# Optimization experiments

Hardware: AMD Instinct MI355X
Metric: run time of the kernel (lower is better)

## Reference

```python
import jax, jax.numpy as jnp
import numpy as np

N_HEADS = 16
HEAD_DIM = 128


def _rotate_half(x):
    x1, x2 = jnp.split(x, 2, axis=-1)
    return jnp.concatenate((-x2, x1), axis=-1)


def setup_inputs() -> dict:
    key = jax.random.key(0)
    ks = jax.random.split(key, 6)
    B, T, D = 2, 2048, 2048
    d = D // N_HEADS  # 128
    x = jax.random.normal(ks[0], (B, T, D), dtype=jnp.float32)
    # RoPE tables (shape [1,1,T,head_dim]) built as in standard implementations
    inv_freq = 1.0 / (10000.0 ** (jnp.arange(0, d, 2, dtype=jnp.float32) / d))
    ang = jnp.arange(T, dtype=jnp.float32)[:, None] * inv_freq[None, :]  # [T, d/2]
    emb = jnp.concatenate((ang, ang), axis=-1)  # [T, d]
    rope_cos = jnp.cos(emb)[None, None]
    rope_sin = jnp.sin(emb)[None, None]
    qkv_w = jax.random.normal(ks[1], (3 * D, D), dtype=jnp.float32) * (1.0 / np.sqrt(D))
    qkv_b = jnp.zeros((3 * D,), dtype=jnp.float32)
    out_w = jax.random.normal(ks[2], (D, D), dtype=jnp.float32) * (1.0 / np.sqrt(D))
    out_b = jnp.zeros((D,), dtype=jnp.float32)
    return {"x": x, "rope_cos": rope_cos, "rope_sin": rope_sin,
            "qkv_w": qkv_w, "qkv_b": qkv_b, "out_w": out_w, "out_b": out_b}


def reference(x, rope_cos, rope_sin, qkv_w, qkv_b, out_w, out_b):
    B, T, D = x.shape
    H, d = N_HEADS, D // N_HEADS
    # fused QKV projection: [B,T,3D] -> [3,B,H,T,d]
    qkv = (jnp.einsum('btd,ed->bte', x, qkv_w) + qkv_b)
    qkv = qkv.reshape(B, T, 3, H, d).transpose(2, 0, 3, 1, 4)
    q, k, v = qkv[0], qkv[1], qkv[2]
    cos = rope_cos[:, :, :T, :].astype(q.dtype)
    sin = rope_sin[:, :, :T, :].astype(q.dtype)
    q = q * cos + _rotate_half(q) * sin
    k = k * cos + _rotate_half(k) * sin
    # causal SDPA
    scale = 1.0 / jnp.sqrt(jnp.array(d, dtype=q.dtype))
    scores = jnp.einsum('bhqd,bhkd->bhqk', q, k) * scale  # [B,H,T,T]
    causal = jnp.tril(jnp.ones((T, T), dtype=bool))
    scores = jnp.where(causal, scores, jnp.finfo(scores.dtype).min)
    attn = jax.nn.softmax(scores, axis=-1)
    out = jnp.einsum('bhqk,bhkd->bhqd', attn, v)  # [B,H,T,d]
    out = out.transpose(0, 2, 1, 3).reshape(B, T, D)
    return jnp.einsum('btd,ed->bte', out, out_w) + out_b
```

## Files before the change

### kernel.cpp

```cpp
#include <hip/hip_runtime.h>
#include <cstdint>
#include <cstddef>

typedef unsigned short u16;
using bf16x8 = __attribute__((ext_vector_type(8))) short;
using f32x4  = __attribute__((ext_vector_type(4))) float;

#define MFMA16(a, b, c) __builtin_amdgcn_mfma_f32_16x16x32_bf16((a), (b), (c), 0, 0, 0)

__device__ __forceinline__ u16 f2bf(float f) {
  union { float f; unsigned u; } x; x.f = f;
  unsigned r = x.u + 0x7fffu + ((x.u >> 16) & 1u);
  return (u16)(r >> 16);
}
__device__ __forceinline__ float bf2f(u16 h) {
  union { unsigned u; float f; } x; x.u = ((unsigned)h) << 16;
  return x.f;
}
__device__ __forceinline__ void gll16(const void* g, void* l) {
  __builtin_amdgcn_global_load_lds((const __attribute__((address_space(1))) void*)g,
                                   (__attribute__((address_space(3))) void*)l, 16, 0, 0);
}

union U8 { bf16x8 v; u16 u[8]; };

__global__ __launch_bounds__(256) void cvt_kernel(const float* __restrict__ in,
                                                  u16* __restrict__ out, int n4) {
  int i = blockIdx.x * blockDim.x + threadIdx.x;
  if (i >= n4) return;
  float4 v = ((const float4*)in)[i];
  ushort4 o;
  o.x = f2bf(v.x); o.y = f2bf(v.y); o.z = f2bf(v.z); o.w = f2bf(v.w);
  ((ushort4*)out)[i] = o;
}

__global__ __launch_bounds__(512, 2) void gemm_bt256(const u16* __restrict__ A,
                                                     const u16* __restrict__ Bw,
                                                     const float* __restrict__ bias,
                                                     void* __restrict__ Cout,
                                                     int M, int N, int K, int out_bf16) {
  __shared__ u16 As_[2][16384];
  __shared__ u16 Bs_[2][16384];
  const int tid = threadIdx.x;
  const int lane = tid & 63, wave = tid >> 6;
  const int col = lane & 15, quad = lane >> 4;
  const int wr = wave >> 2, wc = wave & 3;
  const int bm = blockIdx.y, bn = blockIdx.x;
  const u16* Ag = A + (size_t)bm * 256 * K;
  const u16* Bg = Bw + (size_t)bn * 256 * K;
  const int srow = tid >> 2;
  const int sslot = tid & 3;
  const int ssw = (sslot ^ ((srow >> 1) & 3)) << 3;
  const size_t g0 = (size_t)srow * K + ssw;
  const size_t g1 = (size_t)(srow + 128) * K + ssw;
  const int swq = (quad ^ ((col >> 1) & 3)) << 3;
  const int aro = (wr * 128 + col) * 32 + swq;
  const int bro = (wc * 64 + col) * 32 + swq;
  u16* const As0 = &As_[0][0]; u16* const As1 = &As_[1][0];
  u16* const Bs0 = &Bs_[0][0]; u16* const Bs1 = &Bs_[1][0];
  f32x4 acc[8][4] = {};
  bf16x8 a[8], bq[2];
  const int NI = K >> 7;

#define STG_A(BUF, KS, KT) do { \
    gll16(Ag + g0 + (KT) + (KS) * 32, (void*)((BUF) + (KS) * 8192 + tid * 8)); \
    gll16(Ag + g1 + (KT) + (KS) * 32, (void*)((BUF) + (KS) * 8192 + 4096 + tid * 8)); } while (0)
#define STG_B(BUF, KS, KT) do { \
    gll16(Bg + g0 + (KT) + (KS) * 32, (void*)((BUF) + (KS) * 8192 + tid * 8)); \
    gll16(Bg + g1 + (KT) + (KS) * 32, (void*)((BUF) + (KS) * 8192 + 4096 + tid * 8)); } while (0)
#define RD_A(BUF, KS) do { _Pragma("unroll") \
    for (int m_ = 0; m_ < 8; m_++) \
      a[m_] = *(const bf16x8*)&(BUF)[(KS) * 8192 + aro + m_ * 512]; } while (0)
#define RD_B(BUF, KS, NH) do { _Pragma("unroll") \
    for (int n_ = 0; n_ < 2; n_++) \
      bq[n_] = *(const bf16x8*)&(BUF)[(KS) * 8192 + bro + ((NH) * 2 + n_) * 512]; } while (0)
#define MM(NH) do { _Pragma("unroll") \
    for (int m_ = 0; m_ < 8; m_++) { _Pragma("unroll") \
      for (int n_ = 0; n_ < 2; n_++) \
        acc[m_][(NH) * 2 + n_] = MFMA16(a[m_], bq[n_], acc[m_][(NH) * 2 + n_]); } } while (0)
#define PH(RDS, STGS, MMS, WT) do { \
    RDS; STGS; \
    __builtin_amdgcn_s_barrier(); \
    asm volatile("s_waitcnt lgkmcnt(0)" ::: "memory"); \
    __builtin_amdgcn_s_setprio(1); \
    MMS; \
    __builtin_amdgcn_s_setprio(0); \
    WT; \
    __builtin_amdgcn_s_barrier(); } while (0)
#define VM6 do { asm volatile("s_waitcnt vmcnt(6)" ::: "memory"); } while (0)
#define VM0 do { asm volatile("s_waitcnt vmcnt(0)" ::: "memory"); } while (0)
#define NOPW do { } while (0)

#define ITER(I, LAST) do { \
    const int kt1_ = ((2 * (I) + 1) << 6), kt2_ = kt1_ + 64, kt3_ = kt2_ + 64; \
    PH({ RD_A(As0, 0); RD_B(Bs0, 0, 0); }, { STG_B(Bs1, 1, kt1_); },                MM(0), NOPW); \
    PH({ RD_B(Bs0, 0, 1); },               { if (!(LAST)) STG_A(As0, 0, kt2_); },   MM(1), NOPW); \
    PH({ RD_A(As0, 1); RD_B(Bs0, 1, 1); }, { if (!(LAST)) STG_B(Bs0, 0, kt2_); },   MM(1), NOPW); \
    PH({ RD_B(Bs0, 1, 0); },               { if (!(LAST)) STG_A(As0, 1, kt2_); },   MM(0), \
       if (LAST) { VM0; } else { VM6; }); \
    PH({ RD_A(As1, 0); RD_B(Bs1, 0, 0); }, { if (!(LAST)) STG_B(Bs0, 1, kt2_); },   MM(0), NOPW); \
    PH({ RD_B(Bs1, 0, 1); },               { if (!(LAST)) STG_A(As1, 0, kt3_); },   MM(1), NOPW); \
    PH({ RD_A(As1, 1); RD_B(Bs1, 1, 1); }, { if (!(LAST)) STG_B(Bs1, 0, kt3_); },   MM(1), NOPW); \
    PH({ RD_B(Bs1, 1, 0); },               { if (!(LAST)) STG_A(As1, 1, kt3_); },   MM(0), \
       if (!(LAST)) { VM6; }); \
  } while (0)

  STG_A(As0, 0, 0);  STG_B(Bs0, 0, 0);  STG_A(As0, 1, 0);  STG_B(Bs0, 1, 0);
  STG_A(As1, 0, 64); STG_B(Bs1, 0, 64); STG_A(As1, 1, 64);
  VM6;
  __builtin_amdgcn_s_barrier();

  for (int i = 0; i < NI - 1; ++i) ITER(i, false);
  ITER(NI - 1, true);

#pragma unroll
  for (int i = 0; i < 8; i++) {
    const int row0 = bm * 256 + wr * 128 + i * 16 + quad * 4;
#pragma unroll
    for (int j = 0; j < 4; j++) {
      const int cn = bn * 256 + wc * 64 + j * 16 + col;
      const float bv = bias[cn];
#pragma unroll
      for (int r = 0; r < 4; r++) {
        float v = acc[i][j][r] + bv;
        size_t off = (size_t)(row0 + r) * N + cn;
        if (out_bf16) ((u16*)Cout)[off] = f2bf(v);
        else          ((float*)Cout)[off] = v;
      }
    }
  }
#undef STG_A
#undef STG_B
#undef RD_A
#undef RD_B
#undef MM
#undef PH
#undef VM6
#undef VM0
#undef NOPW
#undef ITER
}

__global__ __launch_bounds__(512, 2) void gemm_bt128(const u16* __restrict__ A,
                                                     const u16* __restrict__ Bw,
                                                     const float* __restrict__ bias,
                                                     void* __restrict__ Cout,
                                                     int M, int N, int K, int out_bf16) {
  __shared__ u16 As_[2][8192];
  __shared__ u16 Bs_[2][16384];
  const int tid = threadIdx.x;
  const int lane = tid & 63, wave = tid >> 6;
  const int col = lane & 15, quad = lane >> 4;
  const int wr = wave >> 2, wc = wave & 3;
  const int bm = blockIdx.y, bn = blockIdx.x;
  const u16* Ag = A + (size_t)bm * 128 * K;
  const u16* Bg = Bw + (size_t)bn * 256 * K;
  const int srow = tid >> 2;
  const int sslot = tid & 3;
  const int ssw = (sslot ^ ((srow >> 1) & 3)) << 3;
  const size_t g0 = (size_t)srow * K + ssw;
  const size_t g1 = (size_t)(srow + 128) * K + ssw;
  const int swq = (quad ^ ((col >> 1) & 3)) << 3;
  const int aro = (wr * 64 + col) * 32 + swq;
  const int bro = (wc * 64 + col) * 32 + swq;
  u16* const As0 = &As_[0][0]; u16* const As1 = &As_[1][0];
  u16* const Bs0 = &Bs_[0][0]; u16* const Bs1 = &Bs_[1][0];
  f32x4 acc[4][4] = {};
  bf16x8 a[4], bq[2];
  const int NI = K >> 7;

#define STG_A(BUF, KS, KT) do { \
    gll16(Ag + g0 + (KT) + (KS) * 32, (void*)((BUF) + (KS) * 4096 + tid * 8)); } while (0)
#define STG_B(BUF, KS, KT) do { \
    gll16(Bg + g0 + (KT) + (KS) * 32, (void*)((BUF) + (KS) * 8192 + tid * 8)); \
    gll16(Bg + g1 + (KT) + (KS) * 32, (void*)((BUF) + (KS) * 8192 + 4096 + tid * 8)); } while (0)
#define RD_A(BUF, KS) do { _Pragma("unroll") \
    for (int m_ = 0; m_ < 4; m_++) \
      a[m_] = *(const bf16x8*)&(BUF)[(KS) * 4096 + aro + m_ * 512]; } while (0)
#define RD_B(BUF, KS, NH) do { _Pragma("unroll") \
    for (int n_ = 0; n_ < 2; n_++) \
      bq[n_] = *(const bf16x8*)&(BUF)[(KS) * 8192 + bro + ((NH) * 2 + n_) * 512]; } while (0)
#define MM(NH) do { _Pragma("unroll") \
    for (int m_ = 0; m_ < 4; m_++) { _Pragma("unroll") \
      for (int n_ = 0; n_ < 2; n_++) \
        acc[m_][(NH) * 2 + n_] = MFMA16(a[m_], bq[n_], acc[m_][(NH) * 2 + n_]); } } while (0)
#define PH(RDS, STGS, MMS, WT) do { \
    RDS; STGS; \
    __builtin_amdgcn_s_barrier(); \
    asm volatile("s_waitcnt lgkmcnt(0)" ::: "memory"); \
    __builtin_amdgcn_s_setprio(1); \
    MMS; \
    __builtin_amdgcn_s_setprio(0); \
    WT; \
    __builtin_amdgcn_s_barrier(); } while (0)
#define VM4 do { asm volatile("s_waitcnt vmcnt(4)" ::: "memory"); } while (0)
#define VM0 do { asm volatile("s_waitcnt vmcnt(0)" ::: "memory"); } while (0)
#define NOPW do { } while (0)

#define ITER(I, LAST) do { \
    const int kt1_ = ((2 * (I) + 1) << 6), kt2_ = kt1_ + 64, kt3_ = kt2_ + 64; \
    PH({ RD_A(As0, 0); RD_B(Bs0, 0, 0); }, { STG_B(Bs1, 1, kt1_); },                MM(0), NOPW); \
    PH({ RD_B(Bs0, 0, 1); },               { if (!(LAST)) STG_A(As0, 0, kt2_); },   MM(1), NOPW); \
    PH({ RD_A(As0, 1); RD_B(Bs0, 1, 1); }, { if (!(LAST)) STG_B(Bs0, 0, kt2_); },   MM(1), NOPW); \
    PH({ RD_B(Bs0, 1, 0); },               { if (!(LAST)) STG_A(As0, 1, kt2_); },   MM(0), \
       if (LAST) { VM0; } else { VM4; }); \
    PH({ RD_A(As1, 0); RD_B(Bs1, 0, 0); }, { if (!(LAST)) STG_B(Bs0, 1, kt2_); },   MM(0), NOPW); \
    PH({ RD_B(Bs1, 0, 1); },               { if (!(LAST)) STG_A(As1, 0, kt3_); },   MM(1), NOPW); \
    PH({ RD_A(As1, 1); RD_B(Bs1, 1, 1); }, { if (!(LAST)) STG_B(Bs1, 0, kt3_); },   MM(1), NOPW); \
    PH({ RD_B(Bs1, 1, 0); },               { if (!(LAST)) STG_A(As1, 1, kt3_); },   MM(0), \
       if (!(LAST)) { VM4; }); \
  } while (0)

  STG_A(As0, 0, 0);  STG_B(Bs0, 0, 0);  STG_A(As0, 1, 0);  STG_B(Bs0, 1, 0);
  STG_A(As1, 0, 64); STG_B(Bs1, 0, 64); STG_A(As1, 1, 64);
  VM4;
  __builtin_amdgcn_s_barrier();

  for (int i = 0; i < NI - 1; ++i) ITER(i, false);
  ITER(NI - 1, true);

#pragma unroll
  for (int i = 0; i < 4; i++) {
    const int row0 = bm * 128 + wr * 64 + i * 16 + quad * 4;
#pragma unroll
    for (int j = 0; j < 4; j++) {
      const int cn = bn * 256 + wc * 64 + j * 16 + col;
      const float bv = bias[cn];
#pragma unroll
      for (int r = 0; r < 4; r++) {
        float v = acc[i][j][r] + bv;
        size_t off = (size_t)(row0 + r) * N + cn;
        if (out_bf16) ((u16*)Cout)[off] = f2bf(v);
        else          ((float*)Cout)[off] = v;
      }
    }
  }
#undef STG_A
#undef STG_B
#undef RD_A
#undef RD_B
#undef MM
#undef PH
#undef VM4
#undef VM0
#undef NOPW
#undef ITER
}

__global__ __launch_bounds__(256) void rope_kernel(const u16* __restrict__ qkv,
                                                   const float* __restrict__ cosT,
                                                   const float* __restrict__ sinT,
                                                   u16* __restrict__ qo,
                                                   u16* __restrict__ ko,
                                                   u16* __restrict__ vt) {
  __shared__ u16 vs[128 * 72];
  const int bh = blockIdx.x;
  const int b = bh >> 4, h = bh & 15;
  const int tb = blockIdx.y;
  const int tid = threadIdx.x;
  const int tl = tid >> 2;
  const int g = tid & 3;
  const int t = tb * 64 + tl;
  const size_t qrow = ((size_t)(b * 2048 + t)) * 6144 + h * 128;
  const size_t orow = ((size_t)bh * 2048 + t) * 128;
  const int tt = t * 128;
  const int dl = g * 16, dh = 64 + dl;
  const float scale = 0.08838834764831845f;
#pragma unroll
  for (int cch = 0; cch < 2; cch++) {
    const int o8 = cch * 8;
    U8 ql, qh, kl, kh, vl, vh;
    ql.v = *(const bf16x8*)&qkv[qrow + dl + o8];
    qh.v = *(const bf16x8*)&qkv[qrow + dh + o8];
    kl.v = *(const bf16x8*)&qkv[qrow + 2048 + dl + o8];
    kh.v = *(const bf16x8*)&qkv[qrow + 2048 + dh + o8];
    vl.v = *(const bf16x8*)&qkv[qrow + 4096 + dl + o8];
    vh.v = *(const bf16x8*)&qkv[qrow + 4096 + dh + o8];
    float cl[8], ch_[8], sl[8], sh_[8];
    *(float4*)&cl[0]  = *(const float4*)&cosT[tt + dl + o8];
    *(float4*)&cl[4]  = *(const float4*)&cosT[tt + dl + o8 + 4];
    *(float4*)&ch_[0] = *(const float4*)&cosT[tt + dh + o8];
    *(float4*)&ch_[4] = *(const float4*)&cosT[tt + dh + o8 + 4];
    *(float4*)&sl[0]  = *(const float4*)&sinT[tt + dl + o8];
    *(float4*)&sl[4]  = *(const float4*)&sinT[tt + dl + o8 + 4];
    *(float4*)&sh_[0] = *(const float4*)&sinT[tt + dh + o8];
    *(float4*)&sh_[4] = *(const float4*)&sinT[tt + dh + o8 + 4];
    U8 aq, bq, ak, bk;
#pragma unroll
    for (int i = 0; i < 8; i++) {
      float qlf = bf2f(ql.u[i]), qhf = bf2f(qh.u[i]);
      float klf = bf2f(kl.u[i]), khf = bf2f(kh.u[i]);
      aq.u[i] = f2bf((qlf * cl[i]  - qhf * sl[i])  * scale);
      bq.u[i] = f2bf((qhf * ch_[i] + qlf * sh_[i]) * scale);
      ak.u[i] = f2bf(klf * cl[i]  - khf * sl[i]);
      bk.u[i] = f2bf(khf * ch_[i] + klf * sh_[i]);
    }
    *(bf16x8*)&qo[orow + dl + o8] = aq.v;
    *(bf16x8*)&qo[orow + dh + o8] = bq.v;
    *(bf16x8*)&ko[orow + dl + o8] = ak.v;
    *(bf16x8*)&ko[orow + dh + o8] = bk.v;
#pragma unroll
    for (int i = 0; i < 8; i++) {
      vs[(dl + o8 + i) * 72 + tl] = vl.u[i];
      vs[(dh + o8 + i) * 72 + tl] = vh.u[i];
    }
  }
  __syncthreads();
#pragma unroll
  for (int c = 0; c < 4; c++) {
    int idx = c * 256 + tid;
    int dd = idx >> 3, chk = idx & 7;
    bf16x8 vv = *(const bf16x8*)&vs[dd * 72 + chk * 8];
    *(bf16x8*)&vt[((size_t)bh * 128 + dd) * 2048 + tb * 64 + chk * 8] = vv;
  }
}

__global__ __launch_bounds__(256) void attn_kernel(const u16* __restrict__ Q,
                                                   const u16* __restrict__ Kk,
                                                   const u16* __restrict__ Vt,
                                                   u16* __restrict__ O) {
  __shared__ u16 Ks[64 * 136];
  __shared__ u16 Vs[128 * 72];
  __shared__ u16 Ps[4][16 * 72];
  const int L = blockIdx.x;
  const int bh = (L < 256) ? (L >> 4) : 16 + ((L - 256) >> 4);
  const int qtile = (L < 256) ? (15 - (L & 15)) : (L & 15);
  const int b = bh >> 4, h = bh & 15;
  const int qb = qtile * 128;
  const int tid = threadIdx.x, wave = tid >> 6, lane = tid & 63;
  const int col = lane & 15, quad = lane >> 4;
  const int qw0 = qb + wave * 32;
  const int qw1 = qw0 + 16;
  const u16* Qg = Q + (size_t)bh * 2048 * 128;
  const u16* Kg = Kk + (size_t)bh * 2048 * 128;
  const u16* Vg = Vt + (size_t)bh * 128 * 2048;
  bf16x8 qf0[4], qf1[4];
#pragma unroll
  for (int c = 0; c < 4; c++) {
    qf0[c] = *(const bf16x8*)&Qg[(size_t)(qw0 + col) * 128 + c * 32 + quad * 8];
    qf1[c] = *(const bf16x8*)&Qg[(size_t)(qw1 + col) * 128 + c * 32 + quad * 8];
  }
  f32x4 o0[8] = {}, o1[8] = {};
  float ls0[4] = {0.f, 0.f, 0.f, 0.f}, ls1[4] = {0.f, 0.f, 0.f, 0.f};
  const int ntiles = (qb + 128) >> 6;
  const int kr = tid >> 2, kc = (tid & 3) * 8;
  const int vr = tid >> 1, vc = (tid & 1) * 8;
  for (int it = 0; it < ntiles; ++it) {
    const int kt = it << 6;
    __syncthreads();
#pragma unroll
    for (int u = 0; u < 4; u++)
      *(bf16x8*)&Ks[kr * 136 + kc + u * 32] =
          *(const bf16x8*)&Kg[(size_t)(kt + kr) * 128 + kc + u * 32];
#pragma unroll
    for (int u = 0; u < 4; u++)
      *(bf16x8*)&Vs[vr * 72 + vc + u * 16] =
          *(const bf16x8*)&Vg[(size_t)vr * 2048 + kt + vc + u * 16];
    __syncthreads();
    if (kt > qw1 + 15) continue;
    const bool do0 = (kt <= qw0 + 15);
    f32x4 s0[4] = {}, s1[4] = {};
#pragma unroll
    for (int c = 0; c < 4; c++) {
#pragma unroll
      for (int kg = 0; kg < 4; kg++) {
        bf16x8 kf = *(const bf16x8*)&Ks[(kg * 16 + col) * 136 + c * 32 + quad * 8];
        s0[kg] = MFMA16(qf0[c], kf, s0[kg]);
        s1[kg] = MFMA16(qf1[c], kf, s1[kg]);
      }
    }
    u16* pw = Ps[wave];
    if (do0) {
#pragma unroll
      for (int kg = 0; kg < 4; kg++)
#pragma unroll
        for (int r = 0; r < 4; r++) {
          int key = kt + kg * 16 + col, qg = qw0 + quad * 4 + r;
          float p = (key <= qg) ? __expf(s0[kg][r]) : 0.f;
          ls0[r] += p;
          pw[(quad * 4 + r) * 72 + kg * 16 + col] = f2bf(p);
        }
#pragma unroll
      for (int ks = 0; ks < 64; ks += 32) {
        bf16x8 pf = *(const bf16x8*)&pw[col * 72 + ks + quad * 8];
#pragma unroll
        for (int dt = 0; dt < 8; dt++) {
          bf16x8 vf = *(const bf16x8*)&Vs[(dt * 16 + col) * 72 + ks + quad * 8];
          o0[dt] = MFMA16(pf, vf, o0[dt]);
        }
      }
    }
    {
#pragma unroll
      for (int kg = 0; kg < 4; kg++)
#pragma unroll
        for (int r = 0; r < 4; r++) {
          int key = kt + kg * 16 + col, qg = qw1 + quad * 4 + r;
          float p = (key <= qg) ? __expf(s1[kg][r]) : 0.f;
          ls1[r] += p;
          pw[(quad * 4 + r) * 72 + kg * 16 + col] = f2bf(p);
        }
#pragma unroll
      for (int ks = 0; ks < 64; ks += 32) {
        bf16x8 pf = *(const bf16x8*)&pw[col * 72 + ks + quad * 8];
#pragma unroll
        for (int dt = 0; dt < 8; dt++) {
          bf16x8 vf = *(const bf16x8*)&Vs[(dt * 16 + col) * 72 + ks + quad * 8];
          o1[dt] = MFMA16(pf, vf, o1[dt]);
        }
      }
    }
  }
#pragma unroll
  for (int st = 1; st < 16; st <<= 1)
#pragma unroll
    for (int r = 0; r < 4; r++) {
      ls0[r] += __shfl_xor(ls0[r], st);
      ls1[r] += __shfl_xor(ls1[r], st);
    }
#pragma unroll
  for (int r = 0; r < 4; r++) {
    float inv0 = 1.0f / ls0[r], inv1 = 1.0f / ls1[r];
    size_t row0 = ((size_t)(b * 2048 + qw0 + quad * 4 + r)) * 2048 + h * 128;
    size_t row1 = ((size_t)(b * 2048 + qw1 + quad * 4 + r)) * 2048 + h * 128;
#pragma unroll
    for (int dt = 0; dt < 8; dt++) {
      O[row0 + dt * 16 + col] = f2bf(o0[dt][r] * inv0);
      O[row1 + dt * 16 + col] = f2bf(o1[dt][r] * inv1);
    }
  }
}

extern "C" void kernel_launch(void* const* d_in, const int* in_sizes, int n_in,
                              void* d_out, int out_size, void* d_ws, size_t ws_size,
                              hipStream_t stream) {
  const float* x        = (const float*)d_in[0];
  const float* rope_cos = (const float*)d_in[1];
  const float* rope_sin = (const float*)d_in[2];
  const float* qkv_w    = (const float*)d_in[3];
  const float* qkv_b    = (const float*)d_in[4];
  const float* out_w    = (const float*)d_in[5];
  const float* out_b    = (const float*)d_in[6];
  float* out = (float*)d_out;
  u16* ws = (u16*)d_ws;
  u16* xb    = ws;
  u16* wqkvb = xb + 8388608;
  u16* woutb = wqkvb + 12582912;
  u16* qkvb  = woutb + 4194304;
  u16* qb    = qkvb + 25165824;
  u16* kb    = qb + 8388608;
  u16* vtb   = kb + 8388608;
  u16* attnb = xb;

  cvt_kernel<<<8192, 256, 0, stream>>>(x, xb, 2097152);
  cvt_kernel<<<12288, 256, 0, stream>>>(qkv_w, wqkvb, 3145728);
  cvt_kernel<<<4096, 256, 0, stream>>>(out_w, woutb, 1048576);
  gemm_bt256<<<dim3(24, 16), 512, 0, stream>>>(xb, wqkvb, qkv_b, qkvb, 4096, 6144, 2048, 1);
  rope_kernel<<<dim3(32, 32), 256, 0, stream>>>(qkvb, rope_cos, rope_sin, qb, kb, vtb);
  attn_kernel<<<dim3(512, 1), 256, 0, stream>>>(qb, kb, vtb, attnb);
  gemm_bt128<<<dim3(8, 32), 512, 0, stream>>>(attnb, woutb, out_b, out, 4096, 2048, 2048, 0);
}
```

Baseline: 430.1 us.

## Swizzle attention LDS layouts, merge PV loops, fuse three convert kernels

Replaces the padded LDS layouts for K, V and P in the attention kernel with XOR-swizzled unpadded layouts to avoid bank conflicts. It gives each query half its own P buffer so both PV products run in one loop that shares each V fragment read. It also merges the three fp32-to-bf16 conversion launches into one kernel to cut launch overhead. The risks are extra index arithmetic and more live registers from the fused PV loop.

```diff
diff --git a/kernel.cpp b/kernel.cpp
--- a/kernel.cpp
+++ b/kernel.cpp
@@ -24,14 +24,23 @@
 
 union U8 { bf16x8 v; u16 u[8]; };
 
-__global__ __launch_bounds__(256) void cvt_kernel(const float* __restrict__ in,
-                                                  u16* __restrict__ out, int n4) {
+__global__ __launch_bounds__(256) void cvt3_kernel(const float* __restrict__ a,
+                                                   const float* __restrict__ b,
+                                                   const float* __restrict__ c,
+                                                   u16* __restrict__ oa,
+                                                   u16* __restrict__ ob,
+                                                   u16* __restrict__ oc,
+                                                   int n1, int n2, int n3) {
   int i = blockIdx.x * blockDim.x + threadIdx.x;
-  if (i >= n4) return;
-  float4 v = ((const float4*)in)[i];
+  const float* src; u16* dst; int j;
+  if (i < n1)            { src = a; dst = oa; j = i; }
+  else if (i < n1 + n2)  { src = b; dst = ob; j = i - n1; }
+  else if (i < n1 + n2 + n3) { src = c; dst = oc; j = i - n1 - n2; }
+  else return;
+  float4 v = ((const float4*)src)[j];
   ushort4 o;
   o.x = f2bf(v.x); o.y = f2bf(v.y); o.z = f2bf(v.z); o.w = f2bf(v.w);
-  ((ushort4*)out)[i] = o;
+  ((ushort4*)dst)[j] = o;
 }
 
 __global__ __launch_bounds__(512, 2) void gemm_bt256(const u16* __restrict__ A,
@@ -319,9 +328,9 @@
                                                    const u16* __restrict__ Kk,
                                                    const u16* __restrict__ Vt,
                                                    u16* __restrict__ O) {
-  __shared__ u16 Ks[64 * 136];
-  __shared__ u16 Vs[128 * 72];
-  __shared__ u16 Ps[4][16 * 72];
+  __shared__ u16 Ks[64 * 128];
+  __shared__ u16 Vs[128 * 64];
+  __shared__ u16 Ps[4][2048];
   const int L = blockIdx.x;
   const int bh = (L < 256) ? (L >> 4) : 16 + ((L - 256) >> 4);
   const int qtile = (L < 256) ? (15 - (L & 15)) : (L & 15);
@@ -343,19 +352,23 @@
   f32x4 o0[8] = {}, o1[8] = {};
   float ls0[4] = {0.f, 0.f, 0.f, 0.f}, ls1[4] = {0.f, 0.f, 0.f, 0.f};
   const int ntiles = (qb + 128) >> 6;
-  const int kr = tid >> 2, kc = (tid & 3) * 8;
-  const int vr = tid >> 1, vc = (tid & 1) * 8;
+  const int skr = tid >> 4, sks = tid & 15;
+  const int svr = tid >> 1, svc = tid & 1;
   for (int it = 0; it < ntiles; ++it) {
     const int kt = it << 6;
     __syncthreads();
 #pragma unroll
-    for (int u = 0; u < 4; u++)
-      *(bf16x8*)&Ks[kr * 136 + kc + u * 32] =
-          *(const bf16x8*)&Kg[(size_t)(kt + kr) * 128 + kc + u * 32];
-#pragma unroll
-    for (int u = 0; u < 4; u++)
-      *(bf16x8*)&Vs[vr * 72 + vc + u * 16] =
-          *(const bf16x8*)&Vg[(size_t)vr * 2048 + kt + vc + u * 16];
+    for (int u = 0; u < 4; u++) {
+      const int row = u * 16 + skr;
+      *(bf16x8*)&Ks[row * 128 + ((sks ^ (row & 7)) << 3)] =
+          *(const bf16x8*)&Kg[(size_t)(kt + row) * 128 + (sks << 3)];
+    }
+#pragma unroll
+    for (int u = 0; u < 4; u++) {
+      const int ch = svc + 2 * u;
+      *(bf16x8*)&Vs[svr * 64 + ((ch ^ (svr & 7)) << 3)] =
+          *(const bf16x8*)&Vg[(size_t)svr * 2048 + kt + (ch << 3)];
+    }
     __syncthreads();
     if (kt > qw1 + 15) continue;
     const bool do0 = (kt <= qw0 + 15);
@@ -364,12 +377,14 @@
     for (int c = 0; c < 4; c++) {
 #pragma unroll
       for (int kg = 0; kg < 4; kg++) {
-        bf16x8 kf = *(const bf16x8*)&Ks[(kg * 16 + col) * 136 + c * 32 + quad * 8];
+        const int krow = kg * 16 + col;
+        bf16x8 kf = *(const bf16x8*)&Ks[krow * 128 + (((c * 4 + quad) ^ (krow & 7)) << 3)];
         s0[kg] = MFMA16(qf0[c], kf, s0[kg]);
         s1[kg] = MFMA16(qf1[c], kf, s1[kg]);
       }
     }
-    u16* pw = Ps[wave];
+    u16* pw0 = &Ps[wave][0];
+    u16* pw1 = &Ps[wave][1024];
     if (do0) {
 #pragma unroll
       for (int kg = 0; kg < 4; kg++)
@@ -378,17 +393,9 @@
           int key = kt + kg * 16 + col, qg = qw0 + quad * 4 + r;
           float p = (key <= qg) ? __expf(s0[kg][r]) : 0.f;
           ls0[r] += p;
-          pw[(quad * 4 + r) * 72 + kg * 16 + col] = f2bf(p);
+          const int prow = quad * 4 + r;
+          pw0[prow * 64 + (((kg * 2 + (col >> 3)) ^ (prow & 7)) << 3) + (col & 7)] = f2bf(p);
         }
-#pragma unroll
-      for (int ks = 0; ks < 64; ks += 32) {
-        bf16x8 pf = *(const bf16x8*)&pw[col * 72 + ks + quad * 8];
-#pragma unroll
-        for (int dt = 0; dt < 8; dt++) {
-          bf16x8 vf = *(const bf16x8*)&Vs[(dt * 16 + col) * 72 + ks + quad * 8];
-          o0[dt] = MFMA16(pf, vf, o0[dt]);
-        }
-      }
     }
     {
 #pragma unroll
@@ -398,16 +405,22 @@
           int key = kt + kg * 16 + col, qg = qw1 + quad * 4 + r;
           float p = (key <= qg) ? __expf(s1[kg][r]) : 0.f;
           ls1[r] += p;
-          pw[(quad * 4 + r) * 72 + kg * 16 + col] = f2bf(p);
+          const int prow = quad * 4 + r;
+          pw1[prow * 64 + (((kg * 2 + (col >> 3)) ^ (prow & 7)) << 3) + (col & 7)] = f2bf(p);
         }
-#pragma unroll
-      for (int ks = 0; ks < 64; ks += 32) {
-        bf16x8 pf = *(const bf16x8*)&pw[col * 72 + ks + quad * 8];
-#pragma unroll
-        for (int dt = 0; dt < 8; dt++) {
-          bf16x8 vf = *(const bf16x8*)&Vs[(dt * 16 + col) * 72 + ks + quad * 8];
-          o1[dt] = MFMA16(pf, vf, o1[dt]);
-        }
+    }
+#pragma unroll
+    for (int ks = 0; ks < 64; ks += 32) {
+      const int cbase = ks >> 3;
+      bf16x8 pf0, pf1;
+      if (do0) pf0 = *(const bf16x8*)&pw0[col * 64 + (((cbase + quad) ^ (col & 7)) << 3)];
+      pf1 = *(const bf16x8*)&pw1[col * 64 + (((cbase + quad) ^ (col & 7)) << 3)];
+#pragma unroll
+      for (int dt = 0; dt < 8; dt++) {
+        const int vrow = dt * 16 + col;
+        bf16x8 vf = *(const bf16x8*)&Vs[vrow * 64 + (((cbase + quad) ^ (vrow & 7)) << 3)];
+        if (do0) o0[dt] = MFMA16(pf0, vf, o0[dt]);
+        o1[dt] = MFMA16(pf1, vf, o1[dt]);
       }
     }
   }
@@ -452,9 +465,8 @@
   u16* vtb   = kb + 8388608;
   u16* attnb = xb;
 
-  cvt_kernel<<<8192, 256, 0, stream>>>(x, xb, 2097152);
-  cvt_kernel<<<12288, 256, 0, stream>>>(qkv_w, wqkvb, 3145728);
-  cvt_kernel<<<4096, 256, 0, stream>>>(out_w, woutb, 1048576);
+  cvt3_kernel<<<24576, 256, 0, stream>>>(x, qkv_w, out_w, xb, wqkvb, woutb,
+                                         2097152, 3145728, 1048576);
   gemm_bt256<<<dim3(24, 16), 512, 0, stream>>>(xb, wqkvb, qkv_b, qkvb, 4096, 6144, 2048, 1);
   rope_kernel<<<dim3(32, 32), 256, 0, stream>>>(qkvb, rope_cos, rope_sin, qb, kb, vtb);
   attn_kernel<<<dim3(512, 1), 256, 0, stream>>>(qb, kb, vtb, attnb);
```

Result: slower. 487.0 us (+13.2%).
